# Performance work log

Measured on AMD Instinct MI355X. Metric: run time of the kernel, lower is better.

Reference implementation:

```python
import jax, jax.numpy as jnp
import numpy as np

B, I, N = 512, 128, 256
ODE_UNFOLDS = 6

def setup_inputs() -> dict:
    key = jax.random.key(0)
    ks = jax.random.split(key, 16)
    u = lambda k, shape, lo, hi: jax.random.uniform(k, shape, jnp.float32, lo, hi)
    inputs = jax.random.normal(ks[0], (B, I), jnp.float32)
    state = jax.random.normal(ks[1], (B, N), jnp.float32)
    sensory_mu = u(ks[2], (I, N), 0.3, 0.8)
    sensory_sigma = u(ks[3], (I, N), 3.0, 8.0)
    sensory_W = u(ks[4], (I, N), 0.01, 1.0)
    sensory_erev = (2.0 * jax.random.randint(ks[5], (I, N), 0, 2).astype(jnp.float32) - 1.0)
    mu = u(ks[6], (N, N), 0.3, 0.8)
    sigma = u(ks[7], (N, N), 3.0, 8.0)
    W = u(ks[8], (N, N), 0.01, 1.0)
    erev = (2.0 * jax.random.randint(ks[9], (N, N), 0, 2).astype(jnp.float32) - 1.0)
    vleak = u(ks[10], (N,), -0.2, 0.2)
    gleak = jnp.ones((N,), jnp.float32)         # gleak_init_min == gleak_init_max == 1.0
    cm_t = jnp.full((N,), 0.5, jnp.float32)     # cm_init_min == cm_init_max == 0.5
    return dict(inputs=inputs, state=state, sensory_mu=sensory_mu,
                sensory_sigma=sensory_sigma, sensory_W=sensory_W,
                sensory_erev=sensory_erev, mu=mu, sigma=sigma, W=W, erev=erev,
                vleak=vleak, gleak=gleak, cm_t=cm_t)

def reference(inputs, state, sensory_mu, sensory_sigma, sensory_W, sensory_erev,
              mu, sigma, W, erev, vleak, gleak, cm_t):
    # sensory gating: (B, I, N)
    s_act = sensory_W * jax.nn.sigmoid(sensory_sigma * (inputs[:, :, None] - sensory_mu))
    w_num_sensory = jnp.sum(s_act * sensory_erev, axis=1)  # (B, N)
    w_den_sensory = jnp.sum(s_act, axis=1)                 # (B, N)

    def step(v_pre, _):
        # recurrent gating: (B, N, N)
        w_act = W * jax.nn.sigmoid(sigma * (v_pre[:, :, None] - mu))
        w_num = jnp.sum(w_act * erev, axis=1) + w_num_sensory
        w_den = jnp.sum(w_act, axis=1) + w_den_sensory
        numerator = cm_t * v_pre + gleak * vleak + w_num
        denominator = cm_t + gleak + w_den
        return numerator / denominator, None

    v, _ = jax.lax.scan(step, state, None, length=ODE_UNFOLDS)
    return (v, v)
```

## Files before the change

kernel.cpp:

```cpp
#include <hip/hip_runtime.h>
#include <stdint.h>

#define NN 256
#define II 128
#define BATCH 512
#define STEPS 6
#define LOG2E 1.4426950408889634f

__device__ __forceinline__ unsigned short f2bf(float x) {
    unsigned u = __builtin_bit_cast(unsigned, x);
    u += 0x7FFFu + ((u >> 16) & 1u);
    return (unsigned short)(u >> 16);
}
__device__ __forceinline__ float bflo(unsigned u) { return __builtin_bit_cast(float, u << 16); }
__device__ __forceinline__ float bfhi(unsigned u) { return __builtin_bit_cast(float, u & 0xFFFF0000u); }

__global__ void pack_weights(const float* __restrict__ sigma, const float* __restrict__ mu,
                             const float* __restrict__ W, const float* __restrict__ erev,
                             unsigned* __restrict__ pq, unsigned* __restrict__ wp, int rows)
{
    int idx = blockIdx.x * blockDim.x + threadIdx.x;
    if (idx >= rows * NN) return;
    int i = idx >> 8, j = idx & (NN - 1);
    float sg = sigma[idx];
    float p = -LOG2E * sg;
    float q =  LOG2E * sg * mu[idx];
    pq[idx] = ((unsigned)f2bf(q) << 16) | (unsigned)f2bf(p);
    if (!(i & 1)) {
        float w0 = W[idx] * erev[idx];
        float w1 = W[idx + NN] * erev[idx + NN];
        wp[(i >> 1) * NN + j] = ((unsigned)f2bf(w1) << 16) | (unsigned)f2bf(w0);
    }
}

template<bool PACKED>
__global__ __launch_bounds__(1024, 4)
void ltc_kernel(const float* __restrict__ inputs, const float* __restrict__ state,
                const float* __restrict__ s_sigma, const float* __restrict__ s_mu,
                const float* __restrict__ s_W, const float* __restrict__ s_erev,
                const float* __restrict__ r_sigma, const float* __restrict__ r_mu,
                const float* __restrict__ r_W, const float* __restrict__ r_erev,
                const unsigned* __restrict__ spq, const unsigned* __restrict__ swp,
                const unsigned* __restrict__ rpq, const unsigned* __restrict__ rwp,
                const float* __restrict__ vleak, const float* __restrict__ gleak,
                const float* __restrict__ cm, float* __restrict__ out)
{
    __shared__ float  v_sh[2][NN];
    __shared__ float  x_sh[2][II];
    __shared__ float2 sens_sh[2][NN];
    __shared__ float2 part[8][NN];

    const int tid  = threadIdx.x;
    const int j    = tid & (NN - 1);
    const int q    = tid >> 8;
    const int row0 = blockIdx.x * 2;

    if (tid < 2 * NN) {
        int r = tid >> 8, c = tid & (NN - 1);
        v_sh[r][c] = state[(row0 + r) * NN + c];
    } else if (tid < 2 * NN + 2 * II) {
        int t = tid - 2 * NN;
        x_sh[t >> 7][t & (II - 1)] = inputs[(row0 + (t >> 7)) * II + (t & (II - 1))];
    }

    const int r2 = tid >> 8;
    float cmv = 0.f, glvl = 0.f, denb = 0.f;
    if (tid < 512) {
        float c = cm[j], g = gleak[j];
        cmv = c; glvl = g * vleak[j]; denb = c + g;
    }
    __syncthreads();

    {
        float sn[2] = {0.f, 0.f}, sd[2] = {0.f, 0.f};
        const int ibase = q * 32;
        #pragma unroll 4
        for (int ip = 0; ip < 16; ++ip) {
            const int i = ibase + ip * 2;
            float p0, q0, p1, q1, w0, w1;
            if (PACKED) {
                unsigned u0 = spq[i * NN + j];
                unsigned u1 = spq[(i + 1) * NN + j];
                unsigned uw = swp[(i >> 1) * NN + j];
                p0 = bflo(u0); q0 = bfhi(u0);
                p1 = bflo(u1); q1 = bfhi(u1);
                w0 = bflo(uw); w1 = bfhi(uw);
            } else {
                int k0 = i * NN + j, k1 = k0 + NN;
                float sg0 = s_sigma[k0], sg1 = s_sigma[k1];
                p0 = -LOG2E * sg0; q0 = LOG2E * sg0 * s_mu[k0];
                p1 = -LOG2E * sg1; q1 = LOG2E * sg1 * s_mu[k1];
                w0 = s_W[k0] * s_erev[k0]; w1 = s_W[k1] * s_erev[k1];
            }
            #pragma unroll
            for (int r = 0; r < 2; ++r) {
                float xa = x_sh[r][i], xb = x_sh[r][i + 1];
                float e0 = __builtin_amdgcn_exp2f(fmaf(p0, xa, q0));
                float e1 = __builtin_amdgcn_exp2f(fmaf(p1, xb, q1));
                float t0 = w0 * __builtin_amdgcn_rcpf(1.f + e0);
                float t1 = w1 * __builtin_amdgcn_rcpf(1.f + e1);
                sn[r] += t0 + t1;
                sd[r] += fabsf(t0) + fabsf(t1);
            }
        }
        part[q * 2 + 0][j] = make_float2(sn[0], sd[0]);
        part[q * 2 + 1][j] = make_float2(sn[1], sd[1]);
    }
    __syncthreads();
    if (tid < 512) {
        float2 a0 = part[0 + r2][j], a1 = part[2 + r2][j], a2 = part[4 + r2][j], a3 = part[6 + r2][j];
        sens_sh[r2][j] = make_float2(a0.x + a1.x + a2.x + a3.x, a0.y + a1.y + a2.y + a3.y);
    }
    __syncthreads();

    for (int step = 0; step < STEPS; ++step) {
        float rn[2] = {0.f, 0.f}, rd[2] = {0.f, 0.f};
        const int ibase = q * 64;
        #pragma unroll 4
        for (int ip = 0; ip < 32; ++ip) {
            const int i = ibase + ip * 2;
            float p0, q0, p1, q1, w0, w1;
            if (PACKED) {
                unsigned u0 = rpq[i * NN + j];
                unsigned u1 = rpq[(i + 1) * NN + j];
                unsigned uw = rwp[(i >> 1) * NN + j];
                p0 = bflo(u0); q0 = bfhi(u0);
                p1 = bflo(u1); q1 = bfhi(u1);
                w0 = bflo(uw); w1 = bfhi(uw);
            } else {
                int k0 = i * NN + j, k1 = k0 + NN;
                float sg0 = r_sigma[k0], sg1 = r_sigma[k1];
                p0 = -LOG2E * sg0; q0 = LOG2E * sg0 * r_mu[k0];
                p1 = -LOG2E * sg1; q1 = LOG2E * sg1 * r_mu[k1];
                w0 = r_W[k0] * r_erev[k0]; w1 = r_W[k1] * r_erev[k1];
            }
            #pragma unroll
            for (int r = 0; r < 2; ++r) {
                float va = v_sh[r][i], vb = v_sh[r][i + 1];
                float e0 = __builtin_amdgcn_exp2f(fmaf(p0, va, q0));
                float e1 = __builtin_amdgcn_exp2f(fmaf(p1, vb, q1));
                float t0 = w0 * __builtin_amdgcn_rcpf(1.f + e0);
                float t1 = w1 * __builtin_amdgcn_rcpf(1.f + e1);
                rn[r] += t0 + t1;
                rd[r] += fabsf(t0) + fabsf(t1);
            }
        }
        part[q * 2 + 0][j] = make_float2(rn[0], rd[0]);
        part[q * 2 + 1][j] = make_float2(rn[1], rd[1]);
        __syncthreads();

        if (tid < 512) {
            float2 a0 = part[0 + r2][j], a1 = part[2 + r2][j], a2 = part[4 + r2][j], a3 = part[6 + r2][j];
            float wn = a0.x + a1.x + a2.x + a3.x + sens_sh[r2][j].x;
            float wd = a0.y + a1.y + a2.y + a3.y + sens_sh[r2][j].y;
            float vp = v_sh[r2][j];
            float vn = (fmaf(cmv, vp, glvl) + wn) * __builtin_amdgcn_rcpf(denb + wd);
            v_sh[r2][j] = vn;
            if (step == STEPS - 1) {
                out[(row0 + r2) * NN + j] = vn;
                out[BATCH * NN + (row0 + r2) * NN + j] = vn;
            }
        }
        __syncthreads();
    }
}

extern "C" void kernel_launch(void* const* d_in, const int* in_sizes, int n_in,
                              void* d_out, int out_size, void* d_ws, size_t ws_size,
                              hipStream_t stream)
{
    const float* inputs  = (const float*)d_in[0];
    const float* state   = (const float*)d_in[1];
    const float* s_mu    = (const float*)d_in[2];
    const float* s_sigma = (const float*)d_in[3];
    const float* s_W     = (const float*)d_in[4];
    const float* s_erev  = (const float*)d_in[5];
    const float* mu      = (const float*)d_in[6];
    const float* sigma   = (const float*)d_in[7];
    const float* W       = (const float*)d_in[8];
    const float* erev    = (const float*)d_in[9];
    const float* vleak   = (const float*)d_in[10];
    const float* gleak   = (const float*)d_in[11];
    const float* cm      = (const float*)d_in[12];
    float* out = (float*)d_out;

    const size_t need = (65536 + 32768 + 32768 + 16384) * sizeof(unsigned);
    if (ws_size >= need) {
        unsigned* rpq = (unsigned*)d_ws;
        unsigned* rwp = rpq + 65536;
        unsigned* spq = rwp + 32768;
        unsigned* swp = spq + 32768;
        pack_weights<<<NN, 256, 0, stream>>>(sigma, mu, W, erev, rpq, rwp, NN);
        pack_weights<<<II, 256, 0, stream>>>(s_sigma, s_mu, s_W, s_erev, spq, swp, II);
        ltc_kernel<true><<<BATCH / 2, 1024, 0, stream>>>(
            inputs, state, s_sigma, s_mu, s_W, s_erev, sigma, mu, W, erev,
            spq, swp, rpq, rwp, vleak, gleak, cm, out);
    } else {
        ltc_kernel<false><<<BATCH / 2, 1024, 0, stream>>>(
            inputs, state, s_sigma, s_mu, s_W, s_erev, sigma, mu, W, erev,
            nullptr, nullptr, nullptr, nullptr, vleak, gleak, cm, out);
    }
}
```

Before: 93.03 us.

## Pack weights into uint4 and share one reciprocal across two sigmoids

The weight packing now writes one 16-byte record per pair of rows: p and q for both rows, signed W*erev, and a precomputed |W*erev|. The packed kernel then issues a single vector load per pair instead of three scalar loads. The inner loop computes one rcp of the product (1+e0)(1+e1) and uses cross-multiplication, with packed v2f FMAs, so two sigmoids need one reciprocal instead of two. This trades transcendental throughput for extra multiplies and adds overflow risk when both exponentials are large: the product can reach infinity and zero out terms that should stay finite.

New measurement: 86.13 us. -7.4%, faster.

```diff
diff --git a/kernel.cpp b/kernel.cpp
--- a/kernel.cpp
+++ b/kernel.cpp
@@ -7,6 +7,8 @@
 #define STEPS 6
 #define LOG2E 1.4426950408889634f
 
+typedef float v2f __attribute__((ext_vector_type(2)));
+
 __device__ __forceinline__ unsigned short f2bf(float x) {
     unsigned u = __builtin_bit_cast(unsigned, x);
     u += 0x7FFFu + ((u >> 16) & 1u);
@@ -15,38 +17,34 @@
 __device__ __forceinline__ float bflo(unsigned u) { return __builtin_bit_cast(float, u << 16); }
 __device__ __forceinline__ float bfhi(unsigned u) { return __builtin_bit_cast(float, u & 0xFFFF0000u); }
 
-__global__ void pack_weights(const float* __restrict__ sigma, const float* __restrict__ mu,
-                             const float* __restrict__ W, const float* __restrict__ erev,
-                             unsigned* __restrict__ pq, unsigned* __restrict__ wp, int rows)
+__global__ void pack4(const float* __restrict__ sigma, const float* __restrict__ mu,
+                      const float* __restrict__ W, const float* __restrict__ erev,
+                      uint4* __restrict__ out, int rows)
 {
     int idx = blockIdx.x * blockDim.x + threadIdx.x;
-    if (idx >= rows * NN) return;
-    int i = idx >> 8, j = idx & (NN - 1);
-    float sg = sigma[idx];
-    float p = -LOG2E * sg;
-    float q =  LOG2E * sg * mu[idx];
-    pq[idx] = ((unsigned)f2bf(q) << 16) | (unsigned)f2bf(p);
-    if (!(i & 1)) {
-        float w0 = W[idx] * erev[idx];
-        float w1 = W[idx + NN] * erev[idx + NN];
-        wp[(i >> 1) * NN + j] = ((unsigned)f2bf(w1) << 16) | (unsigned)f2bf(w0);
-    }
-}
-
-template<bool PACKED>
+    if (idx >= (rows / 2) * NN) return;
+    int ip = idx >> 8, j = idx & (NN - 1);
+    int k0 = (ip * 2) * NN + j, k1 = k0 + NN;
+    float sg0 = sigma[k0], sg1 = sigma[k1];
+    float p0 = -LOG2E * sg0, q0 = LOG2E * sg0 * mu[k0];
+    float p1 = -LOG2E * sg1, q1 = LOG2E * sg1 * mu[k1];
+    float w0 = W[k0] * erev[k0], w1 = W[k1] * erev[k1];
+    uint4 u;
+    u.x = ((unsigned)f2bf(q0) << 16) | (unsigned)f2bf(p0);
+    u.y = ((unsigned)f2bf(q1) << 16) | (unsigned)f2bf(p1);
+    u.z = ((unsigned)f2bf(w1) << 16) | (unsigned)f2bf(w0);
+    u.w = ((unsigned)f2bf(fabsf(w1)) << 16) | (unsigned)f2bf(fabsf(w0));
+    out[idx] = u;
+}
+
 __global__ __launch_bounds__(1024, 4)
-void ltc_kernel(const float* __restrict__ inputs, const float* __restrict__ state,
-                const float* __restrict__ s_sigma, const float* __restrict__ s_mu,
-                const float* __restrict__ s_W, const float* __restrict__ s_erev,
-                const float* __restrict__ r_sigma, const float* __restrict__ r_mu,
-                const float* __restrict__ r_W, const float* __restrict__ r_erev,
-                const unsigned* __restrict__ spq, const unsigned* __restrict__ swp,
-                const unsigned* __restrict__ rpq, const unsigned* __restrict__ rwp,
+void ltc_packed(const float* __restrict__ inputs, const float* __restrict__ state,
+                const uint4* __restrict__ sw4, const uint4* __restrict__ rw4,
                 const float* __restrict__ vleak, const float* __restrict__ gleak,
                 const float* __restrict__ cm, float* __restrict__ out)
 {
-    __shared__ float  v_sh[2][NN];
-    __shared__ float  x_sh[2][II];
+    __shared__ __align__(16) float v_sh[2][NN];
+    __shared__ __align__(16) float x_sh[2][II];
     __shared__ float2 sens_sh[2][NN];
     __shared__ float2 part[8][NN];
 
@@ -72,35 +70,133 @@
     __syncthreads();
 
     {
-        float sn[2] = {0.f, 0.f}, sd[2] = {0.f, 0.f};
-        const int ibase = q * 32;
+        v2f sn[2] = {{0.f,0.f},{0.f,0.f}}, sd[2] = {{0.f,0.f},{0.f,0.f}};
         #pragma unroll 4
         for (int ip = 0; ip < 16; ++ip) {
-            const int i = ibase + ip * 2;
-            float p0, q0, p1, q1, w0, w1;
-            if (PACKED) {
-                unsigned u0 = spq[i * NN + j];
-                unsigned u1 = spq[(i + 1) * NN + j];
-                unsigned uw = swp[(i >> 1) * NN + j];
-                p0 = bflo(u0); q0 = bfhi(u0);
-                p1 = bflo(u1); q1 = bfhi(u1);
-                w0 = bflo(uw); w1 = bfhi(uw);
-            } else {
-                int k0 = i * NN + j, k1 = k0 + NN;
-                float sg0 = s_sigma[k0], sg1 = s_sigma[k1];
-                p0 = -LOG2E * sg0; q0 = LOG2E * sg0 * s_mu[k0];
-                p1 = -LOG2E * sg1; q1 = LOG2E * sg1 * s_mu[k1];
-                w0 = s_W[k0] * s_erev[k0]; w1 = s_W[k1] * s_erev[k1];
-            }
-            #pragma unroll
-            for (int r = 0; r < 2; ++r) {
-                float xa = x_sh[r][i], xb = x_sh[r][i + 1];
-                float e0 = __builtin_amdgcn_exp2f(fmaf(p0, xa, q0));
-                float e1 = __builtin_amdgcn_exp2f(fmaf(p1, xb, q1));
-                float t0 = w0 * __builtin_amdgcn_rcpf(1.f + e0);
-                float t1 = w1 * __builtin_amdgcn_rcpf(1.f + e1);
-                sn[r] += t0 + t1;
-                sd[r] += fabsf(t0) + fabsf(t1);
+            const int i = (q * 16 + ip) * 2;
+            uint4 u = sw4[(q * 16 + ip) * NN + j];
+            v2f p01 = {bflo(u.x), bflo(u.y)};
+            v2f q01 = {bfhi(u.x), bfhi(u.y)};
+            v2f ws  = {bflo(u.z), bfhi(u.z)};
+            v2f wa  = {bflo(u.w), bfhi(u.w)};
+            #pragma unroll
+            for (int r = 0; r < 2; ++r) {
+                v2f x01 = *(const v2f*)(&x_sh[r][i]);
+                v2f arg = __builtin_elementwise_fma(p01, x01, q01);
+                v2f e; e.x = __builtin_amdgcn_exp2f(arg.x); e.y = __builtin_amdgcn_exp2f(arg.y);
+                v2f b = e + 1.0f;
+                float rr = __builtin_amdgcn_rcpf(b.x * b.y);
+                v2f bs = __builtin_shufflevector(b, b, 1, 0);
+                v2f rs = {rr, rr};
+                v2f ms = ws * bs;
+                v2f ma = wa * bs;
+                sn[r] = __builtin_elementwise_fma(ms, rs, sn[r]);
+                sd[r] = __builtin_elementwise_fma(ma, rs, sd[r]);
+            }
+        }
+        part[q * 2 + 0][j] = make_float2(sn[0].x + sn[0].y, sd[0].x + sd[0].y);
+        part[q * 2 + 1][j] = make_float2(sn[1].x + sn[1].y, sd[1].x + sd[1].y);
+    }
+    __syncthreads();
+    if (tid < 512) {
+        float2 a0 = part[0 + r2][j], a1 = part[2 + r2][j], a2 = part[4 + r2][j], a3 = part[6 + r2][j];
+        sens_sh[r2][j] = make_float2(a0.x + a1.x + a2.x + a3.x, a0.y + a1.y + a2.y + a3.y);
+    }
+    __syncthreads();
+
+    for (int step = 0; step < STEPS; ++step) {
+        v2f sn[2] = {{0.f,0.f},{0.f,0.f}}, sd[2] = {{0.f,0.f},{0.f,0.f}};
+        #pragma unroll 4
+        for (int ip = 0; ip < 32; ++ip) {
+            const int i = (q * 32 + ip) * 2;
+            uint4 u = rw4[(q * 32 + ip) * NN + j];
+            v2f p01 = {bflo(u.x), bflo(u.y)};
+            v2f q01 = {bfhi(u.x), bfhi(u.y)};
+            v2f ws  = {bflo(u.z), bfhi(u.z)};
+            v2f wa  = {bflo(u.w), bfhi(u.w)};
+            #pragma unroll
+            for (int r = 0; r < 2; ++r) {
+                v2f v01 = *(const v2f*)(&v_sh[r][i]);
+                v2f arg = __builtin_elementwise_fma(p01, v01, q01);
+                v2f e; e.x = __builtin_amdgcn_exp2f(arg.x); e.y = __builtin_amdgcn_exp2f(arg.y);
+                v2f b = e + 1.0f;
+                float rr = __builtin_amdgcn_rcpf(b.x * b.y);
+                v2f bs = __builtin_shufflevector(b, b, 1, 0);
+                v2f rs = {rr, rr};
+                v2f ms = ws * bs;
+                v2f ma = wa * bs;
+                sn[r] = __builtin_elementwise_fma(ms, rs, sn[r]);
+                sd[r] = __builtin_elementwise_fma(ma, rs, sd[r]);
+            }
+        }
+        part[q * 2 + 0][j] = make_float2(sn[0].x + sn[0].y, sd[0].x + sd[0].y);
+        part[q * 2 + 1][j] = make_float2(sn[1].x + sn[1].y, sd[1].x + sd[1].y);
+        __syncthreads();
+
+        if (tid < 512) {
+            float2 a0 = part[0 + r2][j], a1 = part[2 + r2][j], a2 = part[4 + r2][j], a3 = part[6 + r2][j];
+            float wn = a0.x + a1.x + a2.x + a3.x + sens_sh[r2][j].x;
+            float wd = a0.y + a1.y + a2.y + a3.y + sens_sh[r2][j].y;
+            float vp = v_sh[r2][j];
+            float vn = (fmaf(cmv, vp, glvl) + wn) * __builtin_amdgcn_rcpf(denb + wd);
+            v_sh[r2][j] = vn;
+            if (step == STEPS - 1) {
+                out[(row0 + r2) * NN + j] = vn;
+                out[BATCH * NN + (row0 + r2) * NN + j] = vn;
+            }
+        }
+        __syncthreads();
+    }
+}
+
+__global__ __launch_bounds__(1024, 4)
+void ltc_fallback(const float* __restrict__ inputs, const float* __restrict__ state,
+                  const float* __restrict__ s_sigma, const float* __restrict__ s_mu,
+                  const float* __restrict__ s_W, const float* __restrict__ s_erev,
+                  const float* __restrict__ r_sigma, const float* __restrict__ r_mu,
+                  const float* __restrict__ r_W, const float* __restrict__ r_erev,
+                  const float* __restrict__ vleak, const float* __restrict__ gleak,
+                  const float* __restrict__ cm, float* __restrict__ out)
+{
+    __shared__ float  v_sh[2][NN];
+    __shared__ float  x_sh[2][II];
+    __shared__ float2 sens_sh[2][NN];
+    __shared__ float2 part[8][NN];
+
+    const int tid  = threadIdx.x;
+    const int j    = tid & (NN - 1);
+    const int q    = tid >> 8;
+    const int row0 = blockIdx.x * 2;
+
+    if (tid < 2 * NN) {
+        int r = tid >> 8, c = tid & (NN - 1);
+        v_sh[r][c] = state[(row0 + r) * NN + c];
+    } else if (tid < 2 * NN + 2 * II) {
+        int t = tid - 2 * NN;
+        x_sh[t >> 7][t & (II - 1)] = inputs[(row0 + (t >> 7)) * II + (t & (II - 1))];
+    }
+
+    const int r2 = tid >> 8;
+    float cmv = 0.f, glvl = 0.f, denb = 0.f;
+    if (tid < 512) {
+        float c = cm[j], g = gleak[j];
+        cmv = c; glvl = g * vleak[j]; denb = c + g;
+    }
+    __syncthreads();
+
+    {
+        float sn[2] = {0.f, 0.f}, sd[2] = {0.f, 0.f};
+        for (int ii = 0; ii < 32; ++ii) {
+            const int i = q * 32 + ii;
+            int k = i * NN + j;
+            float sg = s_sigma[k];
+            float p = -LOG2E * sg, qq = LOG2E * sg * s_mu[k];
+            float w = s_W[k] * s_erev[k];
+            #pragma unroll
+            for (int r = 0; r < 2; ++r) {
+                float e = __builtin_amdgcn_exp2f(fmaf(p, x_sh[r][i], qq));
+                float t = w * __builtin_amdgcn_rcpf(1.f + e);
+                sn[r] += t; sd[r] += fabsf(t);
             }
         }
         part[q * 2 + 0][j] = make_float2(sn[0], sd[0]);
@@ -114,39 +210,22 @@
     __syncthreads();
 
     for (int step = 0; step < STEPS; ++step) {
-        float rn[2] = {0.f, 0.f}, rd[2] = {0.f, 0.f};
-        const int ibase = q * 64;
-        #pragma unroll 4
-        for (int ip = 0; ip < 32; ++ip) {
-            const int i = ibase + ip * 2;
-            float p0, q0, p1, q1, w0, w1;
-            if (PACKED) {
-                unsigned u0 = rpq[i * NN + j];
-                unsigned u1 = rpq[(i + 1) * NN + j];
-                unsigned uw = rwp[(i >> 1) * NN + j];
-                p0 = bflo(u0); q0 = bfhi(u0);
-                p1 = bflo(u1); q1 = bfhi(u1);
-                w0 = bflo(uw); w1 = bfhi(uw);
-            } else {
-                int k0 = i * NN + j, k1 = k0 + NN;
-                float sg0 = r_sigma[k0], sg1 = r_sigma[k1];
-                p0 = -LOG2E * sg0; q0 = LOG2E * sg0 * r_mu[k0];
-                p1 = -LOG2E * sg1; q1 = LOG2E * sg1 * r_mu[k1];
-                w0 = r_W[k0] * r_erev[k0]; w1 = r_W[k1] * r_erev[k1];
-            }
-            #pragma unroll
-            for (int r = 0; r < 2; ++r) {
-                float va = v_sh[r][i], vb = v_sh[r][i + 1];
-                float e0 = __builtin_amdgcn_exp2f(fmaf(p0, va, q0));
-                float e1 = __builtin_amdgcn_exp2f(fmaf(p1, vb, q1));
-                float t0 = w0 * __builtin_amdgcn_rcpf(1.f + e0);
-                float t1 = w1 * __builtin_amdgcn_rcpf(1.f + e1);
-                rn[r] += t0 + t1;
-                rd[r] += fabsf(t0) + fabsf(t1);
-            }
-        }
-        part[q * 2 + 0][j] = make_float2(rn[0], rd[0]);
-        part[q * 2 + 1][j] = make_float2(rn[1], rd[1]);
+        float sn[2] = {0.f, 0.f}, sd[2] = {0.f, 0.f};
+        for (int ii = 0; ii < 64; ++ii) {
+            const int i = q * 64 + ii;
+            int k = i * NN + j;
+            float sg = r_sigma[k];
+            float p = -LOG2E * sg, qq = LOG2E * sg * r_mu[k];
+            float w = r_W[k] * r_erev[k];
+            #pragma unroll
+            for (int r = 0; r < 2; ++r) {
+                float e = __builtin_amdgcn_exp2f(fmaf(p, v_sh[r][i], qq));
+                float t = w * __builtin_amdgcn_rcpf(1.f + e);
+                sn[r] += t; sd[r] += fabsf(t);
+            }
+        }
+        part[q * 2 + 0][j] = make_float2(sn[0], sd[0]);
+        part[q * 2 + 1][j] = make_float2(sn[1], sd[1]);
         __syncthreads();
 
         if (tid < 512) {
@@ -184,20 +263,17 @@
     const float* cm      = (const float*)d_in[12];
     float* out = (float*)d_out;
 
-    const size_t need = (65536 + 32768 + 32768 + 16384) * sizeof(unsigned);
+    const size_t need = ((NN / 2) * NN + (II / 2) * NN) * sizeof(uint4);
     if (ws_size >= need) {
-        unsigned* rpq = (unsigned*)d_ws;
-        unsigned* rwp = rpq + 65536;
-        unsigned* spq = rwp + 32768;
-        unsigned* swp = spq + 32768;
-        pack_weights<<<NN, 256, 0, stream>>>(sigma, mu, W, erev, rpq, rwp, NN);
-        pack_weights<<<II, 256, 0, stream>>>(s_sigma, s_mu, s_W, s_erev, spq, swp, II);
-        ltc_kernel<true><<<BATCH / 2, 1024, 0, stream>>>(
+        uint4* rw4 = (uint4*)d_ws;
+        uint4* sw4 = rw4 + (NN / 2) * NN;
+        pack4<<<(NN / 2), 256, 0, stream>>>(sigma, mu, W, erev, rw4, NN);
+        pack4<<<(II / 2), 256, 0, stream>>>(s_sigma, s_mu, s_W, s_erev, sw4, II);
+        ltc_packed<<<BATCH / 2, 1024, 0, stream>>>(inputs, state, sw4, rw4,
+                                                   vleak, gleak, cm, out);
+    } else {
+        ltc_fallback<<<BATCH / 2, 1024, 0, stream>>>(
             inputs, state, s_sigma, s_mu, s_W, s_erev, sigma, mu, W, erev,
-            spq, swp, rpq, rwp, vleak, gleak, cm, out);
-    } else {
-        ltc_kernel<false><<<BATCH / 2, 1024, 0, stream>>>(
-            inputs, state, s_sigma, s_mu, s_W, s_erev, sigma, mu, W, erev,
-            nullptr, nullptr, nullptr, nullptr, vleak, gleak, cm, out);
-    }
-}
+            vleak, gleak, cm, out);
+    }
+}
```
